# Performance work log

Hardware: AMD Instinct MI355X
Metric: run time of the kernel (lower is better)

## Reference

```python
import jax, jax.numpy as jnp
import numpy as np

B, L, D, H = 4, 2048, 1024, 16
HD = D // H


def setup_inputs() -> dict:
    key = jax.random.key(0)
    k1, k2, k3 = jax.random.split(key, 3)
    x = jax.random.normal(k1, (B, L, D), dtype=jnp.float32)
    # causal mask: True means masked (matches masked_fill semantics)
    attn_mask = jnp.triu(jnp.ones((L, L), dtype=bool), k=1)
    # xavier-ish init scale
    w_qkv = jax.random.normal(k2, (D, 3 * D), dtype=jnp.float32) * 0.02
    w_proj = jax.random.normal(k3, (D, D), dtype=jnp.float32) * 0.02
    b_proj = jnp.zeros((D,), dtype=jnp.float32)
    return {"x": x, "attn_mask": attn_mask, "w_qkv": w_qkv, "w_proj": w_proj, "b_proj": b_proj}


def reference(x, attn_mask, w_qkv, w_proj, b_proj):
    b, l, d = x.shape
    h, hd = H, HD
    scale = hd ** -0.5
    qkv = x @ w_qkv                                  # (B, L, 3D)
    qkv = qkv.reshape(b, l, 3, h, hd)
    q = qkv[:, :, 0].transpose(0, 2, 1, 3)           # (B, H, L, hd)
    k = qkv[:, :, 1].transpose(0, 2, 1, 3)
    v = qkv[:, :, 2].transpose(0, 2, 1, 3)
    attn = jnp.einsum('bhqd,bhkd->bhqk', q, k) * scale
    attn = jnp.where(attn_mask[None, None, :, :], -jnp.inf, attn)
    attn = jax.nn.softmax(attn, axis=-1)             # dropout is identity at eval
    out = jnp.einsum('bhqk,bhkd->bhqd', attn, v)     # (B, H, L, hd)
    out = out.transpose(0, 2, 1, 3).reshape(b, l, d)
    return out @ w_proj + b_proj
```

## Files before the change

kernel.cpp:

```cpp
#include <hip/hip_runtime.h>
#include <stdint.h>

#define B_ 4
#define L_ 2048
#define D_ 1024
#define H_ 16
#define HD_ 64
#define M_ (B_*L_)
#define N3_ (3*D_)

typedef _Float16 h8 __attribute__((ext_vector_type(8)));
typedef _Float16 h4v __attribute__((ext_vector_type(4)));
typedef float f4 __attribute__((ext_vector_type(4)));

__device__ __forceinline__ void gload16(const void* g, void* l) {
  __builtin_amdgcn_global_load_lds(
      (const __attribute__((address_space(1))) void*)g,
      (__attribute__((address_space(3))) void*)l, 16, 0, 0);
}

__global__ void k_cvt_f16(const float* __restrict__ in, _Float16* __restrict__ out, int n4) {
  int i = blockIdx.x*blockDim.x + threadIdx.x;
  int st = gridDim.x*blockDim.x;
  for (; i < n4; i += st) {
    float4 v = ((const float4*)in)[i];
    h4v o = { (_Float16)v.x, (_Float16)v.y, (_Float16)v.z, (_Float16)v.w };
    ((h4v*)out)[i] = o;
  }
}

__global__ void k_transpose_f16(const float* __restrict__ in, _Float16* __restrict__ out, int R, int C) {
  __shared__ float tile[32][33];
  int bc = blockIdx.x*32, br = blockIdx.y*32;
  int tx = threadIdx.x, ty = threadIdx.y;
  #pragma unroll
  for (int j = 0; j < 32; j += 8)
    tile[ty+j][tx] = in[(size_t)(br+ty+j)*C + bc+tx];
  __syncthreads();
  #pragma unroll
  for (int j = 0; j < 32; j += 8)
    out[(size_t)(bc+ty+j)*R + br+tx] = (_Float16)tile[tx][ty+j];
}

__global__ __launch_bounds__(256,2)
void k_vtrans(const _Float16* __restrict__ Vi, _Float16* __restrict__ Vo) {
  __shared__ _Float16 T[64*64];
  int bh = blockIdx.x >> 5, lt = blockIdx.x & 31;
  int tid = threadIdx.x;
  const _Float16* src = Vi + ((size_t)bh*L_ + lt*64)*64;
  #pragma unroll
  for (int i = 0; i < 2; ++i) {
    int s = tid + i*256;
    int row = s >> 3;
    int swz = (row & 7) ^ ((row >> 3) & 7);
    int c8 = ((s & 7) ^ swz) * 8;
    gload16(src + row*64 + c8, (char*)T + s*16);
  }
  __syncthreads();
  #pragma unroll
  for (int i = 0; i < 2; ++i) {
    int s = tid + i*256;
    int d = s >> 3, c = s & 7;
    h8 v;
    #pragma unroll
    for (int k = 0; k < 8; ++k) {
      int l = c*8 + k;
      int swz = (l & 7) ^ ((l >> 3) & 7);
      int byteoff = (l*8 + ((d >> 3) ^ swz))*16 + (d & 7)*2;
      v[k] = *(const _Float16*)((const char*)T + byteoff);
    }
    *(h8*)(Vo + ((size_t)bh*64 + d)*L_ + lt*64 + c*8) = v;
  }
}

template<int EPI>
__global__ __launch_bounds__(256,2)
void k_gemm(const _Float16* __restrict__ A, const _Float16* __restrict__ Bt,
            float* __restrict__ Cf, const float* __restrict__ bias,
            _Float16* __restrict__ Qo, _Float16* __restrict__ Ko, _Float16* __restrict__ Vo,
            int N, int K, int nbn) {
  __shared__ _Float16 Al[128*64];
  __shared__ _Float16 Bl[128*64];
  int cpx = gridDim.x >> 3;
  int bid = (blockIdx.x & 7)*cpx + (blockIdx.x >> 3);
  int bm = bid / nbn, bn = bid % nbn;
  int tid = threadIdx.x;
  int lane = tid & 63;
  int wm = tid >> 7, wn = (tid >> 6) & 1;
  int g = lane >> 4, cl = lane & 15;
  f4 acc[4][4] = {};
  const _Float16* Ab = A + (size_t)bm*128*K;
  const _Float16* Bb = Bt + (size_t)bn*128*K;
  int s_row[4], s_off[4];
  #pragma unroll
  for (int i = 0; i < 4; ++i) {
    int s = tid + i*256;
    s_row[i] = s >> 3;
    s_off[i] = ((s & 7) ^ (s_row[i] & 7)) * 8;
  }
  for (int kt = 0; kt < K; kt += 64) {
    #pragma unroll
    for (int i = 0; i < 4; ++i) {
      int s = tid + i*256;
      gload16(Ab + (size_t)s_row[i]*K + kt + s_off[i], (char*)Al + s*16);
      gload16(Bb + (size_t)s_row[i]*K + kt + s_off[i], (char*)Bl + s*16);
    }
    __syncthreads();
    #pragma unroll
    for (int kk = 0; kk < 2; ++kk) {
      h8 af[4], bf[4];
      #pragma unroll
      for (int mi = 0; mi < 4; ++mi) {
        int row = wm*64 + mi*16 + cl;
        int c = (kk*4 + g) ^ (row & 7);
        af[mi] = *(const h8*)((const char*)Al + row*128 + c*16);
      }
      #pragma unroll
      for (int ni = 0; ni < 4; ++ni) {
        int row = wn*64 + ni*16 + cl;
        int c = (kk*4 + g) ^ (row & 7);
        bf[ni] = *(const h8*)((const char*)Bl + row*128 + c*16);
      }
      #pragma unroll
      for (int mi = 0; mi < 4; ++mi)
        #pragma unroll
        for (int ni = 0; ni < 4; ++ni)
          acc[mi][ni] = __builtin_amdgcn_mfma_f32_16x16x32_f16(af[mi], bf[ni], acc[mi][ni], 0, 0, 0);
    }
    __syncthreads();
  }
  if (EPI == 1) {
    float bsv[4];
    #pragma unroll
    for (int ni = 0; ni < 4; ++ni) bsv[ni] = bias[bn*128 + wn*64 + ni*16 + cl];
    #pragma unroll
    for (int mi = 0; mi < 4; ++mi)
      #pragma unroll
      for (int r = 0; r < 4; ++r) {
        int m = bm*128 + wm*64 + mi*16 + g*4 + r;
        float* orow = Cf + (size_t)m*N + bn*128 + wn*64 + cl;
        #pragma unroll
        for (int ni = 0; ni < 4; ++ni)
          orow[ni*16] = acc[mi][ni][r] + bsv[ni];
      }
  } else {
    int region = (bn*128) >> 10;
    _Float16* P = (region == 0) ? Qo : (region == 1) ? Ko : Vo;
    float scl = (region == 0) ? 0.18033688011112042f : 1.0f;
    #pragma unroll
    for (int mi = 0; mi < 4; ++mi)
      #pragma unroll
      for (int r = 0; r < 4; ++r) {
        int m = bm*128 + wm*64 + mi*16 + g*4 + r;
        int b = m >> 11, l = m & 2047;
        #pragma unroll
        for (int ni = 0; ni < 4; ++ni) {
          int n = bn*128 + wn*64 + ni*16 + cl;
          int cc = n & 1023;
          int h = cc >> 6, d = cc & 63;
          P[(((size_t)b*16 + h)*2048 + l)*64 + d] = (_Float16)(acc[mi][ni][r] * scl);
        }
      }
  }
}

__global__ __launch_bounds__(256,2)
void k_attn(const _Float16* __restrict__ Q, const _Float16* __restrict__ K,
            const _Float16* __restrict__ Vt, _Float16* __restrict__ Oo) {
  __shared__ _Float16 Kl[2][64*64];
  __shared__ _Float16 Vl[2][64*64];
  __shared__ _Float16 Pl[4][32*64];
  int bid = blockIdx.x;
  int bh = bid & 63;
  int qt = 15 - (bid >> 6);
  int tid = threadIdx.x, lane = tid & 63, w = tid >> 6;
  int g = lane >> 4, cl = lane & 15;
  int qbase = qt*128;
  int qw = qbase + w*32;
  const _Float16* Qh = Q + (size_t)bh*L_*HD_;
  const _Float16* Kh = K + (size_t)bh*L_*HD_;
  const _Float16* Vh = Vt + (size_t)bh*HD_*L_;
  int srow[2], sc8[2];
  #pragma unroll
  for (int i = 0; i < 2; ++i) {
    int s = tid + i*256;
    srow[i] = s >> 3;
    sc8[i] = ((s & 7) ^ (srow[i] & 7)) * 8;
  }
  char* Pw = (char*)&Pl[w][0];
  int pq = cl*128;
  h8 qf[2][2];
  #pragma unroll
  for (int mi = 0; mi < 2; ++mi)
    #pragma unroll
    for (int kk = 0; kk < 2; ++kk)
      qf[mi][kk] = *(const h8*)(Qh + (size_t)(qw + mi*16 + cl)*64 + kk*32 + g*8);
  f4 oacc[2][4] = {};
  float mrun[2] = {-1e30f, -1e30f}, lrun[2] = {0.f, 0.f};
  int ntiles = (qbase >> 6) + 2;

  auto stage = [&](int t, int buf) {
    int kv0s = t*64;
    #pragma unroll
    for (int i = 0; i < 2; ++i) {
      int s = tid + i*256;
      gload16(Kh + (size_t)(kv0s + srow[i])*64 + sc8[i], (char*)&Kl[buf][0] + s*16);
      gload16(Vh + (size_t)srow[i]*L_ + kv0s + sc8[i], (char*)&Vl[buf][0] + s*16);
    }
  };
  stage(0, 0);
  for (int t = 0; t < ntiles; ++t) {
    __syncthreads();
    if (t + 1 < ntiles) stage(t + 1, (t + 1) & 1);
    int kv0 = t*64;
    if (kv0 <= qw + 31) {
      const char* Kb = (const char*)&Kl[t & 1][0];
      const char* Vb = (const char*)&Vl[t & 1][0];
      f4 st[4][2] = {};
      __builtin_amdgcn_s_setprio(1);
      #pragma unroll
      for (int kk = 0; kk < 2; ++kk) {
        h8 kf[4];
        #pragma unroll
        for (int ni = 0; ni < 4; ++ni) {
          int row = ni*16 + cl;
          int c = (kk*4 + g) ^ (row & 7);
          kf[ni] = *(const h8*)(Kb + row*128 + c*16);
        }
        #pragma unroll
        for (int ni = 0; ni < 4; ++ni)
          #pragma unroll
          for (int mi = 0; mi < 2; ++mi)
            st[ni][mi] = __builtin_amdgcn_mfma_f32_16x16x32_f16(kf[ni], qf[mi][kk], st[ni][mi], 0,0,0);
      }
      __builtin_amdgcn_s_setprio(0);
      bool needm = (kv0 + 63) > qw;
      int srcb = (lane & 48) | ((lane >> 2) & 12);
      #pragma unroll
      for (int mi = 0; mi < 2; ++mi) {
        int qq = qw + mi*16 + cl;
        float p[4][4];
        #pragma unroll
        for (int ni = 0; ni < 4; ++ni)
          #pragma unroll
          for (int rr = 0; rr < 4; ++rr) {
            float v = st[ni][mi][rr];
            if (needm) {
              int kv = kv0 + ni*16 + g*4 + rr;
              if (kv > qq) v = -1e30f;
            }
            p[ni][rr] = v;
          }
        float rm = -1e30f;
        #pragma unroll
        for (int ni = 0; ni < 4; ++ni)
          rm = fmaxf(rm, fmaxf(fmaxf(p[ni][0], p[ni][1]), fmaxf(p[ni][2], p[ni][3])));
        rm = fmaxf(rm, __shfl_xor(rm, 16));
        rm = fmaxf(rm, __shfl_xor(rm, 32));
        float mold = mrun[mi];
        float mnew = fmaxf(mold, rm);
        float corr = exp2f(mold - mnew);
        mrun[mi] = mnew;
        float rs = 0.f;
        #pragma unroll
        for (int ni = 0; ni < 4; ++ni)
          #pragma unroll
          for (int rr = 0; rr < 4; ++rr) {
            float e = exp2f(p[ni][rr] - mnew);
            p[ni][rr] = e;
            rs += e;
          }
        rs += __shfl_xor(rs, 16);
        rs += __shfl_xor(rs, 32);
        lrun[mi] = lrun[mi]*corr + rs;
        float c0 = __shfl(corr, srcb);
        float c1 = __shfl(corr, srcb + 1);
        float c2 = __shfl(corr, srcb + 2);
        float c3 = __shfl(corr, srcb + 3);
        #pragma unroll
        for (int di = 0; di < 4; ++di) {
          oacc[mi][di][0] *= c0; oacc[mi][di][1] *= c1;
          oacc[mi][di][2] *= c2; oacc[mi][di][3] *= c3;
        }
        #pragma unroll
        for (int ni = 0; ni < 4; ++ni) {
          auto lo = __builtin_amdgcn_cvt_pkrtz(p[ni][0], p[ni][1]);
          auto hi = __builtin_amdgcn_cvt_pkrtz(p[ni][2], p[ni][3]);
          uint2 q4;
          q4.x = __builtin_bit_cast(unsigned int, lo);
          q4.y = __builtin_bit_cast(unsigned int, hi);
          int off = pq + mi*2048 + (((ni*2 + (g >> 1)) ^ (cl & 7)) << 4) + (g & 1)*8;
          *(uint2*)(Pw + off) = q4;
        }
      }
      __builtin_amdgcn_s_setprio(1);
      #pragma unroll
      for (int ks = 0; ks < 2; ++ks) {
        h8 pa[2], vf[4];
        #pragma unroll
        for (int mi = 0; mi < 2; ++mi)
          pa[mi] = *(const h8*)(Pw + pq + mi*2048 + (((ks*4 + g) ^ (cl & 7)) << 4));
        #pragma unroll
        for (int di = 0; di < 4; ++di) {
          int row = di*16 + cl;
          int c = (ks*4 + g) ^ (row & 7);
          vf[di] = *(const h8*)(Vb + row*128 + c*16);
        }
        #pragma unroll
        for (int mi = 0; mi < 2; ++mi)
          #pragma unroll
          for (int di = 0; di < 4; ++di)
            oacc[mi][di] = __builtin_amdgcn_mfma_f32_16x16x32_f16(pa[mi], vf[di], oacc[mi][di], 0,0,0);
      }
      __builtin_amdgcn_s_setprio(0);
    }
  }
  int b = bh >> 4, h = bh & 15;
  int srcb = (lane & 48) | ((lane >> 2) & 12);
  #pragma unroll
  for (int mi = 0; mi < 2; ++mi) {
    float inv = 1.0f / lrun[mi];
    float iv[4];
    iv[0] = __shfl(inv, srcb);
    iv[1] = __shfl(inv, srcb + 1);
    iv[2] = __shfl(inv, srcb + 2);
    iv[3] = __shfl(inv, srcb + 3);
    #pragma unroll
    for (int r = 0; r < 4; ++r) {
      int qi = qw + mi*16 + g*4 + r;
      _Float16* orow = Oo + (((size_t)b*L_ + qi)*H_ + h)*HD_ + cl;
      #pragma unroll
      for (int di = 0; di < 4; ++di)
        orow[di*16] = (_Float16)(oacc[mi][di][r] * iv[r]);
    }
  }
}

extern "C" void kernel_launch(void* const* d_in, const int* in_sizes, int n_in,
                              void* d_out, int out_size, void* d_ws, size_t ws_size,
                              hipStream_t stream) {
  const float* x      = (const float*)d_in[0];
  const float* w_qkv  = (const float*)d_in[2];
  const float* w_proj = (const float*)d_in[3];
  const float* b_proj = (const float*)d_in[4];
  float* out = (float*)d_out;
  char* ws = (char*)d_ws;
  _Float16* xh     = (_Float16*)(ws);
  _Float16* wqkvT  = (_Float16*)(ws + 16777216);
  _Float16* wprojT = (_Float16*)(ws + 23068672);
  _Float16* Qb     = (_Float16*)(ws + 25165824);
  _Float16* Kb     = (_Float16*)(ws + 41943040);
  _Float16* Vtmp   = (_Float16*)(ws + 58720256);
  _Float16* Vtb    = xh;
  _Float16* AOb    = Vtmp;

  k_cvt_f16<<<2048, 256, 0, stream>>>(x, xh, (B_*L_*D_)/4);
  k_transpose_f16<<<dim3(N3_/32, D_/32), dim3(32,8), 0, stream>>>(w_qkv, wqkvT, D_, N3_);
  k_transpose_f16<<<dim3(D_/32, D_/32), dim3(32,8), 0, stream>>>(w_proj, wprojT, D_, D_);
  k_gemm<0><<<(M_/128)*(N3_/128), 256, 0, stream>>>(xh, wqkvT, nullptr, nullptr,
                                                    Qb, Kb, Vtmp, N3_, D_, N3_/128);
  k_vtrans<<<2048, 256, 0, stream>>>(Vtmp, Vtb);
  k_attn<<<1024, 256, 0, stream>>>(Qb, Kb, Vtb, AOb);
  k_gemm<1><<<(M_/128)*(D_/128), 256, 0, stream>>>(AOb, wprojT, out, b_proj,
                                                   nullptr, nullptr, nullptr, D_, D_, D_/128);
}
```

Before: 289.5 us.

## Switch attention to 32x32x16 MFMA with register-resident P and lazy rescale

Rewrites the flash-attention inner loop to use 32x32x16 MFMA tiles, with each lane owning one query row. This removes the cross-lane shuffles for row max, sum and correction. The softmax probabilities are repacked in registers with one xor-32 shuffle instead of round-tripping through shared memory, so the Pl buffer and its LDS traffic go away. It also adds a lazy rescale that only updates the running max and the output accumulator when the new max exceeds the old one by a threshold. The costs are higher register pressure and more complex layout logic.

```diff
diff --git a/kernel.cpp b/kernel.cpp
--- a/kernel.cpp
+++ b/kernel.cpp
@@ -12,6 +12,8 @@
 typedef _Float16 h8 __attribute__((ext_vector_type(8)));
 typedef _Float16 h4v __attribute__((ext_vector_type(4)));
 typedef float f4 __attribute__((ext_vector_type(4)));
+typedef float f16v __attribute__((ext_vector_type(16)));
+typedef unsigned int u32x4 __attribute__((ext_vector_type(4)));
 
 __device__ __forceinline__ void gload16(const void* g, void* l) {
   __builtin_amdgcn_global_load_lds(
@@ -169,14 +171,14 @@
             const _Float16* __restrict__ Vt, _Float16* __restrict__ Oo) {
   __shared__ _Float16 Kl[2][64*64];
   __shared__ _Float16 Vl[2][64*64];
-  __shared__ _Float16 Pl[4][32*64];
   int bid = blockIdx.x;
   int bh = bid & 63;
   int qt = 15 - (bid >> 6);
   int tid = threadIdx.x, lane = tid & 63, w = tid >> 6;
-  int g = lane >> 4, cl = lane & 15;
+  int l31 = lane & 31, hf = lane >> 5;
   int qbase = qt*128;
   int qw = qbase + w*32;
+  int q = qw + l31;
   const _Float16* Qh = Q + (size_t)bh*L_*HD_;
   const _Float16* Kh = K + (size_t)bh*L_*HD_;
   const _Float16* Vh = Vt + (size_t)bh*HD_*L_;
@@ -187,16 +189,12 @@
     srow[i] = s >> 3;
     sc8[i] = ((s & 7) ^ (srow[i] & 7)) * 8;
   }
-  char* Pw = (char*)&Pl[w][0];
-  int pq = cl*128;
-  h8 qf[2][2];
-  #pragma unroll
-  for (int mi = 0; mi < 2; ++mi)
-    #pragma unroll
-    for (int kk = 0; kk < 2; ++kk)
-      qf[mi][kk] = *(const h8*)(Qh + (size_t)(qw + mi*16 + cl)*64 + kk*32 + g*8);
-  f4 oacc[2][4] = {};
-  float mrun[2] = {-1e30f, -1e30f}, lrun[2] = {0.f, 0.f};
+  h8 qf[4];
+  #pragma unroll
+  for (int kd = 0; kd < 4; ++kd)
+    qf[kd] = *(const h8*)(Qh + (size_t)q*64 + kd*16 + hf*8);
+  f16v oacc[2] = {};
+  float mrun = -1e30f, lrun = 0.f;
   int ntiles = (qbase >> 6) + 2;
 
   auto stage = [&](int t, int buf) {
@@ -216,124 +214,102 @@
     if (kv0 <= qw + 31) {
       const char* Kb = (const char*)&Kl[t & 1][0];
       const char* Vb = (const char*)&Vl[t & 1][0];
-      f4 st[4][2] = {};
+      f16v st[2] = {};
       __builtin_amdgcn_s_setprio(1);
       #pragma unroll
-      for (int kk = 0; kk < 2; ++kk) {
-        h8 kf[4];
-        #pragma unroll
-        for (int ni = 0; ni < 4; ++ni) {
-          int row = ni*16 + cl;
-          int c = (kk*4 + g) ^ (row & 7);
-          kf[ni] = *(const h8*)(Kb + row*128 + c*16);
-        }
-        #pragma unroll
-        for (int ni = 0; ni < 4; ++ni)
-          #pragma unroll
-          for (int mi = 0; mi < 2; ++mi)
-            st[ni][mi] = __builtin_amdgcn_mfma_f32_16x16x32_f16(kf[ni], qf[mi][kk], st[ni][mi], 0,0,0);
-      }
+      for (int kb = 0; kb < 2; ++kb)
+        #pragma unroll
+        for (int kd = 0; kd < 4; ++kd) {
+          int r = kb*32 + l31;
+          int c = (kd*2 + hf) ^ (r & 7);
+          h8 kf = *(const h8*)(Kb + r*128 + c*16);
+          st[kb] = __builtin_amdgcn_mfma_f32_32x32x16_f16(kf, qf[kd], st[kb], 0, 0, 0);
+        }
       __builtin_amdgcn_s_setprio(0);
       bool needm = (kv0 + 63) > qw;
-      int srcb = (lane & 48) | ((lane >> 2) & 12);
-      #pragma unroll
-      for (int mi = 0; mi < 2; ++mi) {
-        int qq = qw + mi*16 + cl;
-        float p[4][4];
-        #pragma unroll
-        for (int ni = 0; ni < 4; ++ni)
+      float p[2][16];
+      #pragma unroll
+      for (int kb = 0; kb < 2; ++kb)
+        #pragma unroll
+        for (int rg = 0; rg < 16; ++rg) {
+          float v = st[kb][rg];
+          if (needm) {
+            int kv = kv0 + kb*32 + (rg & 3) + 8*(rg >> 2) + 4*hf;
+            if (kv > q) v = -1e30f;
+          }
+          p[kb][rg] = v;
+        }
+      float rm = -1e30f;
+      #pragma unroll
+      for (int kb = 0; kb < 2; ++kb)
+        #pragma unroll
+        for (int rg = 0; rg < 16; ++rg) rm = fmaxf(rm, p[kb][rg]);
+      rm = fmaxf(rm, __shfl_xor(rm, 32));
+      if (!__all(rm <= mrun + 8.f)) {
+        float mnew = fmaxf(mrun, rm);
+        float corr = exp2f(mrun - mnew);
+        mrun = mnew;
+        lrun *= corr;
+        #pragma unroll
+        for (int db = 0; db < 2; ++db)
           #pragma unroll
-          for (int rr = 0; rr < 4; ++rr) {
-            float v = st[ni][mi][rr];
-            if (needm) {
-              int kv = kv0 + ni*16 + g*4 + rr;
-              if (kv > qq) v = -1e30f;
-            }
-            p[ni][rr] = v;
-          }
-        float rm = -1e30f;
-        #pragma unroll
-        for (int ni = 0; ni < 4; ++ni)
-          rm = fmaxf(rm, fmaxf(fmaxf(p[ni][0], p[ni][1]), fmaxf(p[ni][2], p[ni][3])));
-        rm = fmaxf(rm, __shfl_xor(rm, 16));
-        rm = fmaxf(rm, __shfl_xor(rm, 32));
-        float mold = mrun[mi];
-        float mnew = fmaxf(mold, rm);
-        float corr = exp2f(mold - mnew);
-        mrun[mi] = mnew;
-        float rs = 0.f;
-        #pragma unroll
-        for (int ni = 0; ni < 4; ++ni)
-          #pragma unroll
-          for (int rr = 0; rr < 4; ++rr) {
-            float e = exp2f(p[ni][rr] - mnew);
-            p[ni][rr] = e;
-            rs += e;
-          }
-        rs += __shfl_xor(rs, 16);
-        rs += __shfl_xor(rs, 32);
-        lrun[mi] = lrun[mi]*corr + rs;
-        float c0 = __shfl(corr, srcb);
-        float c1 = __shfl(corr, srcb + 1);
-        float c2 = __shfl(corr, srcb + 2);
-        float c3 = __shfl(corr, srcb + 3);
-        #pragma unroll
-        for (int di = 0; di < 4; ++di) {
-          oacc[mi][di][0] *= c0; oacc[mi][di][1] *= c1;
-          oacc[mi][di][2] *= c2; oacc[mi][di][3] *= c3;
-        }
-        #pragma unroll
-        for (int ni = 0; ni < 4; ++ni) {
-          auto lo = __builtin_amdgcn_cvt_pkrtz(p[ni][0], p[ni][1]);
-          auto hi = __builtin_amdgcn_cvt_pkrtz(p[ni][2], p[ni][3]);
-          uint2 q4;
-          q4.x = __builtin_bit_cast(unsigned int, lo);
-          q4.y = __builtin_bit_cast(unsigned int, hi);
-          int off = pq + mi*2048 + (((ni*2 + (g >> 1)) ^ (cl & 7)) << 4) + (g & 1)*8;
-          *(uint2*)(Pw + off) = q4;
-        }
+          for (int rg = 0; rg < 16; ++rg) oacc[db][rg] *= corr;
+      }
+      float rs = 0.f;
+      #pragma unroll
+      for (int kb = 0; kb < 2; ++kb)
+        #pragma unroll
+        for (int rg = 0; rg < 16; ++rg) {
+          float e = exp2f(p[kb][rg] - mrun);
+          p[kb][rg] = e;
+          rs += e;
+        }
+      rs += __shfl_xor(rs, 32);
+      lrun += rs;
+      h8 pb[4];
+      #pragma unroll
+      for (int blk = 0; blk < 4; ++blk) {
+        int kb = blk >> 1, sb = (blk & 1)*8;
+        unsigned dw0 = __builtin_bit_cast(unsigned, __builtin_amdgcn_cvt_pkrtz(p[kb][sb+0], p[kb][sb+1]));
+        unsigned dw1 = __builtin_bit_cast(unsigned, __builtin_amdgcn_cvt_pkrtz(p[kb][sb+2], p[kb][sb+3]));
+        unsigned dw2 = __builtin_bit_cast(unsigned, __builtin_amdgcn_cvt_pkrtz(p[kb][sb+4], p[kb][sb+5]));
+        unsigned dw3 = __builtin_bit_cast(unsigned, __builtin_amdgcn_cvt_pkrtz(p[kb][sb+6], p[kb][sb+7]));
+        unsigned eu = hf ? dw0 : dw2;
+        unsigned ev = hf ? dw1 : dw3;
+        unsigned up = (unsigned)__shfl_xor((int)eu, 32);
+        unsigned vp = (unsigned)__shfl_xor((int)ev, 32);
+        u32x4 tmp;
+        if (hf == 0) tmp = (u32x4){dw0, dw1, up, vp};
+        else         tmp = (u32x4){up, vp, dw2, dw3};
+        pb[blk] = __builtin_bit_cast(h8, tmp);
       }
       __builtin_amdgcn_s_setprio(1);
       #pragma unroll
-      for (int ks = 0; ks < 2; ++ks) {
-        h8 pa[2], vf[4];
-        #pragma unroll
-        for (int mi = 0; mi < 2; ++mi)
-          pa[mi] = *(const h8*)(Pw + pq + mi*2048 + (((ks*4 + g) ^ (cl & 7)) << 4));
-        #pragma unroll
-        for (int di = 0; di < 4; ++di) {
-          int row = di*16 + cl;
-          int c = (ks*4 + g) ^ (row & 7);
-          vf[di] = *(const h8*)(Vb + row*128 + c*16);
-        }
-        #pragma unroll
-        for (int mi = 0; mi < 2; ++mi)
-          #pragma unroll
-          for (int di = 0; di < 4; ++di)
-            oacc[mi][di] = __builtin_amdgcn_mfma_f32_16x16x32_f16(pa[mi], vf[di], oacc[mi][di], 0,0,0);
-      }
+      for (int db = 0; db < 2; ++db)
+        #pragma unroll
+        for (int ks = 0; ks < 4; ++ks) {
+          int r = db*32 + l31;
+          int c = (ks*2 + hf) ^ (r & 7);
+          h8 vf = *(const h8*)(Vb + r*128 + c*16);
+          oacc[db] = __builtin_amdgcn_mfma_f32_32x32x16_f16(vf, pb[ks], oacc[db], 0, 0, 0);
+        }
       __builtin_amdgcn_s_setprio(0);
     }
   }
-  int b = bh >> 4, h = bh & 15;
-  int srcb = (lane & 48) | ((lane >> 2) & 12);
-  #pragma unroll
-  for (int mi = 0; mi < 2; ++mi) {
-    float inv = 1.0f / lrun[mi];
-    float iv[4];
-    iv[0] = __shfl(inv, srcb);
-    iv[1] = __shfl(inv, srcb + 1);
-    iv[2] = __shfl(inv, srcb + 2);
-    iv[3] = __shfl(inv, srcb + 3);
-    #pragma unroll
-    for (int r = 0; r < 4; ++r) {
-      int qi = qw + mi*16 + g*4 + r;
-      _Float16* orow = Oo + (((size_t)b*L_ + qi)*H_ + h)*HD_ + cl;
-      #pragma unroll
-      for (int di = 0; di < 4; ++di)
-        orow[di*16] = (_Float16)(oacc[mi][di][r] * iv[r]);
-    }
-  }
+  float inv = 1.0f / lrun;
+  int b = bh >> 4, hh = bh & 15;
+  _Float16* obase = Oo + (((size_t)b*L_ + q)*H_ + hh)*HD_;
+  #pragma unroll
+  for (int db = 0; db < 2; ++db)
+    #pragma unroll
+    for (int grp = 0; grp < 4; ++grp) {
+      unsigned lo = __builtin_bit_cast(unsigned,
+          __builtin_amdgcn_cvt_pkrtz(oacc[db][grp*4+0]*inv, oacc[db][grp*4+1]*inv));
+      unsigned hi = __builtin_bit_cast(unsigned,
+          __builtin_amdgcn_cvt_pkrtz(oacc[db][grp*4+2]*inv, oacc[db][grp*4+3]*inv));
+      uint2 qq; qq.x = lo; qq.y = hi;
+      *(uint2*)(obase + db*32 + grp*8 + 4*hf) = qq;
+    }
 }
 
 extern "C" void kernel_launch(void* const* d_in, const int* in_sizes, int n_in,
```

New measurement: 274.4 us. -5.2%, faster.
